# Kernel optimization log

Measured on AMD Instinct MI355X. Metric: run time of the kernel, lower is better.

The kernel has to match this reference:

```python
import jax, jax.numpy as jnp
import numpy as np

E, TOPK, H, I = 8, 2, 2048, 5632
T = 4096


def setup_inputs() -> dict:
    key = jax.random.key(0)
    k1, k2, k3, k4 = jax.random.split(key, 4)
    hidden_states = jax.random.normal(k1, (T, H), dtype=jnp.float32)
    gate_w = jax.random.normal(k2, (E, H), dtype=jnp.float32) * (1.0 / np.sqrt(H))
    # fused gate+up projection: [E, 2*I, H]
    w13 = jax.random.normal(k3, (E, 2 * I, H), dtype=jnp.float32) * (1.0 / np.sqrt(H))
    # down projection: [E, H, I]
    w2 = jax.random.normal(k4, (E, H, I), dtype=jnp.float32) * (1.0 / np.sqrt(I))
    return {"hidden_states": hidden_states, "gate_w": gate_w, "w13": w13, "w2": w2, "top_k": TOPK}


def reference(hidden_states, gate_w, w13, w2, top_k):
    num_experts = gate_w.shape[0]
    inter = w2.shape[2]
    # router: fp32 gate logits -> softmax -> top-k -> renormalize (FusedMoE renormalize=True)
    logits = hidden_states.astype(jnp.float32) @ gate_w.T          # [T, E]
    probs = jax.nn.softmax(logits, axis=-1)
    vals, idx = jax.lax.top_k(probs, top_k)                        # [T, k]
    vals = vals / jnp.sum(vals, axis=-1, keepdims=True)
    # dense routing weight matrix [T, E] (zero outside top-k)
    dense_w = jnp.sum(jax.nn.one_hot(idx, num_experts, dtype=vals.dtype) * vals[..., None], axis=1)

    def body(acc, inputs):
        w13_e, w2_e, we = inputs                                   # [2I,H], [H,I], [T]
        gu = hidden_states @ w13_e.T                               # [T, 2I]
        g, u = gu[:, :inter], gu[:, inter:]
        h = jax.nn.silu(g) * u                                     # SwiGLU
        y = h @ w2_e.T                                             # [T, H]
        return acc + we[:, None] * y, None

    acc0 = jnp.zeros_like(hidden_states)
    out, _ = jax.lax.scan(body, acc0, (w13, w2, dense_w.T))
    return out
```

## Files before the change

### kernel.cpp

```cpp
#include <hip/hip_runtime.h>

#define T_TOK 4096
#define H_DIM 2048
#define I_DIM 5632
#define NE 8

typedef _Float16 f16;
typedef _Float16 f16x8 __attribute__((ext_vector_type(8)));
typedef float f32x4 __attribute__((ext_vector_type(4)));

#define OFF_META   0
#define OFF_BTOK   256
#define OFF_BW     (256 + 32768)
#define OFF_RE     (256 + 2 * 32768)
#define OFF_RW     (256 + 3 * 32768)
#define OFF_HSB    (256 + 4 * 32768)
#define OFF_WF     (OFF_HSB + (size_t)T_TOK * H_DIM * 2)

typedef const __attribute__((address_space(1))) unsigned int guint;
typedef __attribute__((address_space(3))) unsigned int luint;

__device__ __forceinline__ int swzk(int r, int bir) {
    return (bir & 15) | ((((bir >> 4) ^ r) & 7) << 4);
}

__global__ void cvt_w_kernel(const float* __restrict__ src, f16* __restrict__ dst, int n8) {
    int stride = gridDim.x * blockDim.x;
    for (int i = blockIdx.x * blockDim.x + threadIdx.x; i < n8; i += stride) {
        size_t b = (size_t)i * 8;
        float4 a = *(const float4*)(src + b);
        float4 c = *(const float4*)(src + b + 4);
        f16x8 v;
        v[0] = (f16)a.x; v[1] = (f16)a.y; v[2] = (f16)a.z; v[3] = (f16)a.w;
        v[4] = (f16)c.x; v[5] = (f16)c.y; v[6] = (f16)c.z; v[7] = (f16)c.w;
        *(f16x8*)(dst + b) = v;
    }
}

__global__ void cvt_hs_kernel(const float* __restrict__ hs, f16* __restrict__ hsb) {
    size_t i = ((size_t)blockIdx.x * 256 + threadIdx.x) * 8;
    float4 a = *(const float4*)(hs + i);
    float4 b = *(const float4*)(hs + i + 4);
    f16x8 v;
    v[0] = (f16)a.x; v[1] = (f16)a.y; v[2] = (f16)a.z; v[3] = (f16)a.w;
    v[4] = (f16)b.x; v[5] = (f16)b.y; v[6] = (f16)b.z; v[7] = (f16)b.w;
    *(f16x8*)(hsb + i) = v;
}

__global__ void gate_kernel(const float* __restrict__ hs, const float* __restrict__ gw,
                            int* __restrict__ re, float* __restrict__ rw,
                            int* __restrict__ counts) {
    int lane = threadIdx.x & 63;
    int t = blockIdx.x * 4 + (threadIdx.x >> 6);
    float acc[NE];
#pragma unroll
    for (int e = 0; e < NE; ++e) acc[e] = 0.f;
    const float* x = hs + (size_t)t * H_DIM;
    for (int i = lane; i < H_DIM; i += 64) {
        float xv = x[i];
#pragma unroll
        for (int e = 0; e < NE; ++e) acc[e] += xv * gw[e * H_DIM + i];
    }
#pragma unroll
    for (int e = 0; e < NE; ++e)
        for (int off = 32; off > 0; off >>= 1) acc[e] += __shfl_xor(acc[e], off);
    if (lane == 0) {
        int i1 = 0; float l1 = acc[0];
#pragma unroll
        for (int e = 1; e < NE; ++e) if (acc[e] > l1) { l1 = acc[e]; i1 = e; }
        int i2 = -1; float l2 = -1e30f;
#pragma unroll
        for (int e = 0; e < NE; ++e) if (e != i1 && acc[e] > l2) { l2 = acc[e]; i2 = e; }
        float aa = __expf(l2 - l1);
        float s = 1.f / (1.f + aa);
        re[t * 2] = i1; re[t * 2 + 1] = i2;
        rw[t * 2] = s;  rw[t * 2 + 1] = aa * s;
        atomicAdd(&counts[i1], 1);
        atomicAdd(&counts[i2], 1);
    }
}

__global__ void scan_kernel(int* __restrict__ meta) {
    if (threadIdx.x == 0) {
        int s = 0;
        for (int e = 0; e < NE; ++e) { meta[8 + e] = s; meta[16 + e] = s; s += meta[e]; }
    }
}

__global__ void place_kernel(const int* __restrict__ re, const float* __restrict__ rw,
                             int* __restrict__ cursor, int* __restrict__ btok,
                             float* __restrict__ bwv) {
    int t = blockIdx.x * 256 + threadIdx.x;
    if (t >= T_TOK) return;
#pragma unroll
    for (int s = 0; s < 2; ++s) {
        int e = re[t * 2 + s];
        int p = atomicAdd(&cursor[e], 1);
        btok[p] = t;
        bwv[p] = rw[t * 2 + s];
    }
}

__device__ __forceinline__ void decode_panel(int id, int npx, int e_arg,
                                             int& e, int& bx, int& by) {
    if (e_arg >= 0) { e = e_arg; bx = id >> 5; by = id & 31; return; }
    int sg  = id >> 8;
    int rem = id & 255;
    by = rem >> 3;
    int P = sg * 8 + (rem & 7);
    e = P / npx; bx = P % npx;
}

__global__ __launch_bounds__(256, 4) void gemm1_kernel(
    const f16* __restrict__ w13f, const f16* __restrict__ hsb, f16* __restrict__ hb,
    const int* __restrict__ counts, const int* __restrict__ offs,
    const int* __restrict__ btok,
    const float* __restrict__ w2src, f16* __restrict__ w2dst, int cvt_n8, int cvt_blocks,
    int e_arg, int global_h)
{
    if ((int)blockIdx.x < cvt_blocks) {
        int stride = cvt_blocks * 256;
        for (int i = blockIdx.x * 256 + threadIdx.x; i < cvt_n8; i += stride) {
            size_t b = (size_t)i * 8;
            float4 a = *(const float4*)(w2src + b);
            float4 c = *(const float4*)(w2src + b + 4);
            f16x8 v;
            v[0] = (f16)a.x; v[1] = (f16)a.y; v[2] = (f16)a.z; v[3] = (f16)a.w;
            v[4] = (f16)c.x; v[5] = (f16)c.y; v[6] = (f16)c.z; v[7] = (f16)c.w;
            *(f16x8*)(w2dst + b) = v;
        }
        return;
    }
    int e, bx, by;
    decode_panel((int)blockIdx.x - cvt_blocks, 88, e_arg, e, bx, by);
    const int n_e = counts[e];
    if (by * 128 >= n_e) return;
    const int boff = offs[e];
    const f16* We = (e_arg >= 0) ? w13f : (w13f + (size_t)e * (2 * I_DIM) * H_DIM);

    const int tid = threadIdx.x;
    const int lane = tid & 63;
    const int wid = tid >> 6;
    const int wm = wid >> 1, wn = wid & 1;
    const int l15 = lane & 15;

    __shared__ f16 As[128 * 64];
    __shared__ f16 Bs[128 * 64];

    const f16* gA[4]; const f16* gB[4]; int dstc[4];
#pragma unroll
    for (int i = 0; i < 4; ++i) {
        int c = i * 256 + tid;
        int r = c >> 3;
        dstc[i] = c * 16;
        int slot = ((c & 7) ^ (r & 7)) * 8;
        int idx = by * 128 + r;
        idx = idx < n_e ? idx : n_e - 1;
        gA[i] = hsb + (size_t)btok[boff + idx] * H_DIM + slot;
        int wrow = (r < 64) ? (bx * 64 + r) : (I_DIM + bx * 64 + (r - 64));
        gB[i] = We + (size_t)wrow * H_DIM + slot;
    }

    f32x4 ag[4][2], au[4][2];
#pragma unroll
    for (int m = 0; m < 4; ++m)
#pragma unroll
        for (int n = 0; n < 2; ++n) { ag[m][n] = (f32x4)0.f; au[m][n] = (f32x4)0.f; }

    const int NT = H_DIM / 64;

#pragma unroll 1
    for (int kt = 0; kt < NT; ++kt) {
        __syncthreads();
        const int k0 = kt * 64;
#pragma unroll
        for (int i = 0; i < 4; ++i) {
            __builtin_amdgcn_global_load_lds((guint*)(gA[i] + k0), (luint*)((char*)As + dstc[i]), 16, 0, 0);
            __builtin_amdgcn_global_load_lds((guint*)(gB[i] + k0), (luint*)((char*)Bs + dstc[i]), 16, 0, 0);
        }
        __syncthreads();
#pragma unroll
        for (int kh = 0; kh < 2; ++kh) {
            const int kb = kh * 64 + (lane >> 4) * 16;
            f16x8 a[4], bg[2], bu[2];
#pragma unroll
            for (int m = 0; m < 4; ++m) {
                int r = wm * 64 + m * 16 + l15;
                a[m] = *(const f16x8*)((const char*)As + r * 128 + swzk(r, kb));
            }
#pragma unroll
            for (int n = 0; n < 2; ++n) {
                int rg = wn * 32 + n * 16 + l15;
                bg[n] = *(const f16x8*)((const char*)Bs + rg * 128 + swzk(rg, kb));
                int ru = 64 + rg;
                bu[n] = *(const f16x8*)((const char*)Bs + ru * 128 + swzk(ru, kb));
            }
#pragma unroll
            for (int m = 0; m < 4; ++m)
#pragma unroll
                for (int n = 0; n < 2; ++n) {
                    ag[m][n] = __builtin_amdgcn_mfma_f32_16x16x32_f16(a[m], bg[n], ag[m][n], 0, 0, 0);
                    au[m][n] = __builtin_amdgcn_mfma_f32_16x16x32_f16(a[m], bu[n], au[m][n], 0, 0, 0);
                }
        }
    }

    const int hbase = (global_h ? boff : 0) + by * 128;
#pragma unroll
    for (int m = 0; m < 4; ++m) {
        int rl0 = wm * 64 + m * 16 + ((lane >> 4) << 2);
#pragma unroll
        for (int r = 0; r < 4; ++r) {
            int rl = rl0 + r;
            if (by * 128 + rl < n_e) {
#pragma unroll
                for (int n = 0; n < 2; ++n) {
                    float g = ag[m][n][r];
                    float u = au[m][n][r];
                    float h = g / (1.f + __expf(-g)) * u;
                    hb[(size_t)(hbase + rl) * I_DIM + bx * 64 + wn * 32 + n * 16 + l15] = (f16)h;
                }
            }
        }
    }
}

__global__ __launch_bounds__(256, 4) void gemm2_kernel(
    const f16* __restrict__ w2f, const f16* __restrict__ hb, float* __restrict__ out,
    const int* __restrict__ counts, const int* __restrict__ offs,
    const int* __restrict__ btok, const float* __restrict__ bwv, int e_arg, int global_h)
{
    int e, bx, by;
    decode_panel(blockIdx.x, 16, e_arg, e, bx, by);
    const int n_e = counts[e];
    if (by * 128 >= n_e) return;
    const int boff = offs[e];
    const f16* We = (e_arg >= 0) ? w2f : (w2f + (size_t)e * H_DIM * I_DIM);

    const int tid = threadIdx.x;
    const int lane = tid & 63;
    const int wid = tid >> 6;
    const int wm = wid >> 1, wn = wid & 1;
    const int l15 = lane & 15;

    __shared__ f16 As[128 * 64];
    __shared__ f16 Bs[128 * 64];

    const int hb0 = global_h ? boff : 0;
    const f16* gA[4]; const f16* gB[4]; int dstc[4];
#pragma unroll
    for (int i = 0; i < 4; ++i) {
        int c = i * 256 + tid;
        int r = c >> 3;
        dstc[i] = c * 16;
        int slot = ((c & 7) ^ (r & 7)) * 8;
        int idx = by * 128 + r;
        idx = idx < n_e ? idx : n_e - 1;
        gA[i] = hb + (size_t)(hb0 + idx) * I_DIM + slot;
        gB[i] = We + (size_t)(bx * 128 + r) * I_DIM + slot;
    }

    f32x4 acc[4][4];
#pragma unroll
    for (int m = 0; m < 4; ++m)
#pragma unroll
        for (int n = 0; n < 4; ++n) acc[m][n] = (f32x4)0.f;

    const int NT = I_DIM / 64;

#pragma unroll 1
    for (int kt = 0; kt < NT; ++kt) {
        __syncthreads();
        const int k0 = kt * 64;
#pragma unroll
        for (int i = 0; i < 4; ++i) {
            __builtin_amdgcn_global_load_lds((guint*)(gA[i] + k0), (luint*)((char*)As + dstc[i]), 16, 0, 0);
            __builtin_amdgcn_global_load_lds((guint*)(gB[i] + k0), (luint*)((char*)Bs + dstc[i]), 16, 0, 0);
        }
        __syncthreads();
#pragma unroll
        for (int kh = 0; kh < 2; ++kh) {
            const int kb = kh * 64 + (lane >> 4) * 16;
            f16x8 a[4], b[4];
#pragma unroll
            for (int m = 0; m < 4; ++m) {
                int r = wm * 64 + m * 16 + l15;
                a[m] = *(const f16x8*)((const char*)As + r * 128 + swzk(r, kb));
            }
#pragma unroll
            for (int n = 0; n < 4; ++n) {
                int r = wn * 64 + n * 16 + l15;
                b[n] = *(const f16x8*)((const char*)Bs + r * 128 + swzk(r, kb));
            }
#pragma unroll
            for (int m = 0; m < 4; ++m)
#pragma unroll
                for (int n = 0; n < 4; ++n)
                    acc[m][n] = __builtin_amdgcn_mfma_f32_16x16x32_f16(a[m], b[n], acc[m][n], 0, 0, 0);
        }
    }

#pragma unroll
    for (int m = 0; m < 4; ++m) {
        int rl0 = wm * 64 + m * 16 + ((lane >> 4) << 2);
#pragma unroll
        for (int r = 0; r < 4; ++r) {
            int rl = rl0 + r;
            if (by * 128 + rl < n_e) {
                int p = boff + by * 128 + rl;
                int tok = btok[p];
                float w = bwv[p];
#pragma unroll
                for (int n = 0; n < 4; ++n)
                    atomicAdd(&out[(size_t)tok * H_DIM + bx * 128 + wn * 64 + n * 16 + l15],
                              w * acc[m][n][r]);
            }
        }
    }
}

extern "C" void kernel_launch(void* const* d_in, const int* in_sizes, int n_in,
                              void* d_out, int out_size, void* d_ws, size_t ws_size,
                              hipStream_t stream) {
    const float* hs  = (const float*)d_in[0];
    const float* gw  = (const float*)d_in[1];
    const float* w13 = (const float*)d_in[2];
    const float* w2  = (const float*)d_in[3];
    float* out = (float*)d_out;

    char* ws = (char*)d_ws;
    int*   meta = (int*)(ws + OFF_META);
    int*   btok = (int*)(ws + OFF_BTOK);
    float* bwv  = (float*)(ws + OFF_BW);
    int*   re   = (int*)(ws + OFF_RE);
    float* rw   = (float*)(ws + OFF_RW);
    f16*   hsb  = (f16*)(ws + OFF_HSB);

    hipMemsetAsync(d_out, 0, (size_t)T_TOK * H_DIM * 4, stream);
    hipMemsetAsync(meta, 0, 256, stream);

    cvt_hs_kernel<<<(T_TOK * H_DIM) / (256 * 8), 256, 0, stream>>>(hs, hsb);
    gate_kernel<<<T_TOK / 4, 256, 0, stream>>>(hs, gw, re, rw, meta);
    scan_kernel<<<1, 64, 0, stream>>>(meta);
    place_kernel<<<T_TOK / 256, 256, 0, stream>>>(re, rw, meta + 16, btok, bwv);

    const size_t w13_elems = (size_t)NE * 2 * I_DIM * H_DIM;
    const size_t w2_elems  = (size_t)NE * H_DIM * I_DIM;

    size_t o_w13f = OFF_WF;
    size_t o_w2f  = o_w13f + w13_elems * 2;
    size_t o_hb   = o_w2f + w2_elems * 2;
    size_t need_full = o_hb + (size_t)2 * T_TOK * I_DIM * 2;

    size_t f_w13 = OFF_WF;
    size_t f_w2  = f_w13 + (size_t)2 * I_DIM * H_DIM * 2;
    size_t f_hb  = f_w2 + (size_t)H_DIM * I_DIM * 2;

    if (ws_size >= need_full) {
        f16* w13f = (f16*)(ws + o_w13f);
        f16* w2f  = (f16*)(ws + o_w2f);
        f16* hb   = (f16*)(ws + o_hb);
        cvt_w_kernel<<<4096, 256, 0, stream>>>(w13, w13f, (int)(w13_elems / 8));
        gemm1_kernel<<<2048 + 704 * 32, 256, 0, stream>>>(
            w13f, hsb, hb, meta, meta + 8, btok,
            w2, w2f, (int)(w2_elems / 8), 2048, -1, 1);
        gemm2_kernel<<<128 * 32, 256, 0, stream>>>(w2f, hb, out, meta, meta + 8, btok, bwv, -1, 1);
    } else {
        f16* w13f = (f16*)(ws + f_w13);
        f16* w2f  = (f16*)(ws + f_w2);
        f16* hb   = (f16*)(ws + f_hb);
        const size_t w13_slice = (size_t)2 * I_DIM * H_DIM;
        const size_t w2_slice  = (size_t)H_DIM * I_DIM;
        for (int e = 0; e < NE; ++e) {
            cvt_w_kernel<<<2048, 256, 0, stream>>>(w13 + e * w13_slice, w13f, (int)(w13_slice / 8));
            gemm1_kernel<<<2048 + 88 * 32, 256, 0, stream>>>(
                w13f, hsb, hb, meta, meta + 8, btok,
                w2 + e * w2_slice, w2f, (int)(w2_slice / 8), 2048, e, 0);
            gemm2_kernel<<<16 * 32, 256, 0, stream>>>(w2f, hb, out, meta, meta + 8, btok, bwv, e, 0);
        }
    }
}
```

Measured before the change: 1.169 ms.

## Replace atomic scatter-add with per-slot stores plus weighted reduce; merge prep kernels

The down-projection GEMM now writes each routed slot's fp32 result to a dense per-slot buffer, and a new reduce kernel combines each token's two weighted expert outputs. This removes the float atomics and the output memset. The weight conversion, hidden-state conversion and gating are also merged into one prep kernel, so they share a launch and can overlap. The cost is an extra 64 MB intermediate write and read plus one more kernel.

```diff
diff --git a/kernel.cpp b/kernel.cpp
--- a/kernel.cpp
+++ b/kernel.cpp
@@ -14,7 +14,8 @@
 #define OFF_BW     (256 + 32768)
 #define OFF_RE     (256 + 2 * 32768)
 #define OFF_RW     (256 + 3 * 32768)
-#define OFF_HSB    (256 + 4 * 32768)
+#define OFF_TP     (256 + 4 * 32768)
+#define OFF_HSB    (256 + 5 * 32768)
 #define OFF_WF     (OFF_HSB + (size_t)T_TOK * H_DIM * 2)
 
 typedef const __attribute__((address_space(1))) unsigned int guint;
@@ -37,21 +38,44 @@
     }
 }
 
-__global__ void cvt_hs_kernel(const float* __restrict__ hs, f16* __restrict__ hsb) {
-    size_t i = ((size_t)blockIdx.x * 256 + threadIdx.x) * 8;
-    float4 a = *(const float4*)(hs + i);
-    float4 b = *(const float4*)(hs + i + 4);
-    f16x8 v;
-    v[0] = (f16)a.x; v[1] = (f16)a.y; v[2] = (f16)a.z; v[3] = (f16)a.w;
-    v[4] = (f16)b.x; v[5] = (f16)b.y; v[6] = (f16)b.z; v[7] = (f16)b.w;
-    *(f16x8*)(hsb + i) = v;
-}
-
-__global__ void gate_kernel(const float* __restrict__ hs, const float* __restrict__ gw,
+__global__ void prep_kernel(const float* __restrict__ w13, f16* __restrict__ w13f, int n8_w13,
+                            int cvt13_b,
+                            const float* __restrict__ hs, f16* __restrict__ hsb,
+                            const float* __restrict__ gw,
                             int* __restrict__ re, float* __restrict__ rw,
                             int* __restrict__ counts) {
+    int id = blockIdx.x;
+    if (id < cvt13_b) {
+        int stride = cvt13_b * 256;
+        for (int i = id * 256 + threadIdx.x; i < n8_w13; i += stride) {
+            size_t b = (size_t)i * 8;
+            float4 a = *(const float4*)(w13 + b);
+            float4 c = *(const float4*)(w13 + b + 4);
+            f16x8 v;
+            v[0] = (f16)a.x; v[1] = (f16)a.y; v[2] = (f16)a.z; v[3] = (f16)a.w;
+            v[4] = (f16)c.x; v[5] = (f16)c.y; v[6] = (f16)c.z; v[7] = (f16)c.w;
+            *(f16x8*)(w13f + b) = v;
+        }
+        return;
+    }
+    id -= cvt13_b;
+    if (id < 1024) {
+        const int n8 = T_TOK * H_DIM / 8;
+        int stride = 1024 * 256;
+        for (int i = id * 256 + threadIdx.x; i < n8; i += stride) {
+            size_t b = (size_t)i * 8;
+            float4 a = *(const float4*)(hs + b);
+            float4 c = *(const float4*)(hs + b + 4);
+            f16x8 v;
+            v[0] = (f16)a.x; v[1] = (f16)a.y; v[2] = (f16)a.z; v[3] = (f16)a.w;
+            v[4] = (f16)c.x; v[5] = (f16)c.y; v[6] = (f16)c.z; v[7] = (f16)c.w;
+            *(f16x8*)(hsb + b) = v;
+        }
+        return;
+    }
+    id -= 1024;
     int lane = threadIdx.x & 63;
-    int t = blockIdx.x * 4 + (threadIdx.x >> 6);
+    int t = id * 4 + (threadIdx.x >> 6);
     float acc[NE];
 #pragma unroll
     for (int e = 0; e < NE; ++e) acc[e] = 0.f;
@@ -89,7 +113,7 @@
 
 __global__ void place_kernel(const int* __restrict__ re, const float* __restrict__ rw,
                              int* __restrict__ cursor, int* __restrict__ btok,
-                             float* __restrict__ bwv) {
+                             float* __restrict__ bwv, int* __restrict__ tpos) {
     int t = blockIdx.x * 256 + threadIdx.x;
     if (t >= T_TOK) return;
 #pragma unroll
@@ -98,6 +122,7 @@
         int p = atomicAdd(&cursor[e], 1);
         btok[p] = t;
         bwv[p] = rw[t * 2 + s];
+        tpos[t * 2 + s] = p;
     }
 }
 
@@ -226,9 +251,9 @@
 }
 
 __global__ __launch_bounds__(256, 4) void gemm2_kernel(
-    const f16* __restrict__ w2f, const f16* __restrict__ hb, float* __restrict__ out,
+    const f16* __restrict__ w2f, const f16* __restrict__ hb, float* __restrict__ y,
     const int* __restrict__ counts, const int* __restrict__ offs,
-    const int* __restrict__ btok, const float* __restrict__ bwv, int e_arg, int global_h)
+    const int* __restrict__ btok, int e_arg, int global_h)
 {
     int e, bx, by;
     decode_panel(blockIdx.x, 16, e_arg, e, bx, by);
@@ -308,14 +333,30 @@
             int rl = rl0 + r;
             if (by * 128 + rl < n_e) {
                 int p = boff + by * 128 + rl;
-                int tok = btok[p];
-                float w = bwv[p];
 #pragma unroll
                 for (int n = 0; n < 4; ++n)
-                    atomicAdd(&out[(size_t)tok * H_DIM + bx * 128 + wn * 64 + n * 16 + l15],
-                              w * acc[m][n][r]);
-            }
-        }
+                    y[(size_t)p * H_DIM + bx * 128 + wn * 64 + n * 16 + l15] = acc[m][n][r];
+            }
+        }
+    }
+}
+
+__global__ void reduce_kernel(const float* __restrict__ y, const int* __restrict__ tpos,
+                              const float* __restrict__ bwv, float* __restrict__ out) {
+    int t = blockIdx.x;
+    int p0 = tpos[t * 2], p1 = tpos[t * 2 + 1];
+    float w0 = bwv[p0], w1 = bwv[p1];
+    const float4* y0 = (const float4*)(y + (size_t)p0 * H_DIM);
+    const float4* y1 = (const float4*)(y + (size_t)p1 * H_DIM);
+    float4* o = (float4*)(out + (size_t)t * H_DIM);
+    for (int i = threadIdx.x; i < H_DIM / 4; i += 256) {
+        float4 a = y0[i], b = y1[i];
+        float4 r;
+        r.x = w0 * a.x + w1 * b.x;
+        r.y = w0 * a.y + w1 * b.y;
+        r.z = w0 * a.z + w1 * b.z;
+        r.w = w0 * a.w + w1 * b.w;
+        o[i] = r;
     }
 }
 
@@ -334,15 +375,10 @@
     float* bwv  = (float*)(ws + OFF_BW);
     int*   re   = (int*)(ws + OFF_RE);
     float* rw   = (float*)(ws + OFF_RW);
+    int*   tpos = (int*)(ws + OFF_TP);
     f16*   hsb  = (f16*)(ws + OFF_HSB);
 
-    hipMemsetAsync(d_out, 0, (size_t)T_TOK * H_DIM * 4, stream);
     hipMemsetAsync(meta, 0, 256, stream);
-
-    cvt_hs_kernel<<<(T_TOK * H_DIM) / (256 * 8), 256, 0, stream>>>(hs, hsb);
-    gate_kernel<<<T_TOK / 4, 256, 0, stream>>>(hs, gw, re, rw, meta);
-    scan_kernel<<<1, 64, 0, stream>>>(meta);
-    place_kernel<<<T_TOK / 256, 256, 0, stream>>>(re, rw, meta + 16, btok, bwv);
 
     const size_t w13_elems = (size_t)NE * 2 * I_DIM * H_DIM;
     const size_t w2_elems  = (size_t)NE * H_DIM * I_DIM;
@@ -350,25 +386,37 @@
     size_t o_w13f = OFF_WF;
     size_t o_w2f  = o_w13f + w13_elems * 2;
     size_t o_hb   = o_w2f + w2_elems * 2;
-    size_t need_full = o_hb + (size_t)2 * T_TOK * I_DIM * 2;
+    size_t o_y    = o_hb + (size_t)2 * T_TOK * I_DIM * 2;
+    size_t need_full = o_y + (size_t)2 * T_TOK * H_DIM * 4;
 
     size_t f_w13 = OFF_WF;
     size_t f_w2  = f_w13 + (size_t)2 * I_DIM * H_DIM * 2;
     size_t f_hb  = f_w2 + (size_t)H_DIM * I_DIM * 2;
+    size_t f_y   = f_hb + (size_t)T_TOK * I_DIM * 2;
 
     if (ws_size >= need_full) {
         f16* w13f = (f16*)(ws + o_w13f);
         f16* w2f  = (f16*)(ws + o_w2f);
         f16* hb   = (f16*)(ws + o_hb);
-        cvt_w_kernel<<<4096, 256, 0, stream>>>(w13, w13f, (int)(w13_elems / 8));
+        float* y  = (float*)(ws + o_y);
+        prep_kernel<<<3072 + 1024 + 1024, 256, 0, stream>>>(
+            w13, w13f, (int)(w13_elems / 8), 3072, hs, hsb, gw, re, rw, meta);
+        scan_kernel<<<1, 64, 0, stream>>>(meta);
+        place_kernel<<<T_TOK / 256, 256, 0, stream>>>(re, rw, meta + 16, btok, bwv, tpos);
         gemm1_kernel<<<2048 + 704 * 32, 256, 0, stream>>>(
             w13f, hsb, hb, meta, meta + 8, btok,
             w2, w2f, (int)(w2_elems / 8), 2048, -1, 1);
-        gemm2_kernel<<<128 * 32, 256, 0, stream>>>(w2f, hb, out, meta, meta + 8, btok, bwv, -1, 1);
+        gemm2_kernel<<<128 * 32, 256, 0, stream>>>(w2f, hb, y, meta, meta + 8, btok, -1, 1);
+        reduce_kernel<<<T_TOK, 256, 0, stream>>>(y, tpos, bwv, out);
     } else {
         f16* w13f = (f16*)(ws + f_w13);
         f16* w2f  = (f16*)(ws + f_w2);
         f16* hb   = (f16*)(ws + f_hb);
+        float* y  = (float*)(ws + f_y);
+        prep_kernel<<<1024 + 1024, 256, 0, stream>>>(
+            w13, (f16*)nullptr, 0, 0, hs, hsb, gw, re, rw, meta);
+        scan_kernel<<<1, 64, 0, stream>>>(meta);
+        place_kernel<<<T_TOK / 256, 256, 0, stream>>>(re, rw, meta + 16, btok, bwv, tpos);
         const size_t w13_slice = (size_t)2 * I_DIM * H_DIM;
         const size_t w2_slice  = (size_t)H_DIM * I_DIM;
         for (int e = 0; e < NE; ++e) {
@@ -376,7 +424,8 @@
             gemm1_kernel<<<2048 + 88 * 32, 256, 0, stream>>>(
                 w13f, hsb, hb, meta, meta + 8, btok,
                 w2 + e * w2_slice, w2f, (int)(w2_slice / 8), 2048, e, 0);
-            gemm2_kernel<<<16 * 32, 256, 0, stream>>>(w2f, hb, out, meta, meta + 8, btok, bwv, e, 0);
-        }
-    }
-}
+            gemm2_kernel<<<16 * 32, 256, 0, stream>>>(w2f, hb, y, meta, meta + 8, btok, e, 0);
+        }
+        reduce_kernel<<<T_TOK, 256, 0, stream>>>(y, tpos, bwv, out);
+    }
+}
```

Result: faster. 1.136 ms (-2.9%).
